# Optimization experiments

Measured on AMD Instinct MI355X. Metric: run time of the kernel, lower is better.

Reference implementation:

```python
import jax, jax.numpy as jnp
import numpy as np

MAX_REL = 64  # max_relative_position
LN_EPS = 1e-5


def _relative_positions(seq_len):
    r = jnp.arange(seq_len)
    rel = jnp.clip(r[None, :] - r[:, None], -MAX_REL, MAX_REL) + MAX_REL
    return rel  # [S, S] int32 in [0, 2*MAX_REL]


def setup_inputs() -> dict:
    key = jax.random.key(0)
    ks = jax.random.split(key, 8)
    B, S, H = 8, 1024, 128
    sd = 1.0 / np.sqrt(H)
    return {
        "x": jax.random.normal(ks[0], (B, S, H), jnp.float32),
        "Wq": jax.random.normal(ks[1], (H, H), jnp.float32) * sd,
        "bq": jnp.zeros((H,), jnp.float32),
        "Wk": jax.random.normal(ks[2], (H, H), jnp.float32) * sd,
        "bk": jnp.zeros((H,), jnp.float32),
        "Wv": jax.random.normal(ks[3], (H, H), jnp.float32) * sd,
        "bv": jnp.zeros((H,), jnp.float32),
        "rel_k": jax.random.normal(ks[4], (2 * MAX_REL + 1, H), jnp.float32),
        "rel_v": jax.random.normal(ks[5], (2 * MAX_REL + 1, H), jnp.float32),
        "Wo": jax.random.normal(ks[6], (H, H), jnp.float32) * sd,
        "bo": jnp.zeros((H,), jnp.float32),
        "gamma": jnp.ones((H,), jnp.float32),
        "beta": jnpp if False else jnp.zeros((H,), jnp.float32),
    }


def reference(x, Wq, bq, Wk, bk, Wv, bv, rel_k, rel_v, Wo, bo, gamma, beta):
    B, S, H = x.shape
    scale = jnp.sqrt(jnp.asarray(H, x.dtype))

    q = x @ Wq + bq  # [B,S,H]
    k = x @ Wk + bk
    v = x @ Wv + bv

    scores = jnp.einsum("bih,bjh->bij", q, k) / scale  # [B,S,S]

    relpos = _relative_positions(S)            # [S,S] int
    rk = rel_k[relpos]                          # [S,S,H] gather
    scores = scores + jnp.einsum("bih,ijh->bij", q, rk)

    attn = jax.nn.softmax(scores, axis=-1)      # dropout = identity (eval)

    ctx = jnp.einsum("bij,bjh->bih", attn, v)
    rv = rel_v[relpos]                          # [S,S,H] gather
    ctx = ctx + jnp.einsum("bij,ijh->bih", attn, rv)

    out = ctx @ Wo + bo

    # residual + LayerNorm
    y = out + x
    mu = jnp.mean(y, axis=-1, keepdims=True)
    var = jnp.mean(jnp.square(y - mu), axis=-1, keepdims=True)
    y = (y - mu) * jax.lax.rsqrt(var + LN_EPS) * gamma + beta
    return y, attn
```

## Files before the change

kernel.cpp:

```cpp
#include <hip/hip_runtime.h>

constexpr int Bn = 8, Sn = 1024, Hn = 128, Rn = 129;
constexpr float INV_SCALE = 0.088388347648318447f;
constexpr size_t YEL = (size_t)Bn * Sn * Hn;

typedef short bf16x8 __attribute__((ext_vector_type(8)));
typedef short v4s __attribute__((ext_vector_type(4)));
typedef float f32x4 __attribute__((ext_vector_type(4)));
typedef int v4i __attribute__((ext_vector_type(4)));

__device__ __forceinline__ float bf2f(short s) {
    unsigned u = ((unsigned)(unsigned short)s) << 16;
    float f; __builtin_memcpy(&f, &u, 4); return f;
}
__device__ __forceinline__ short f2bf(float f) {
    unsigned u; __builtin_memcpy(&u, &f, 4);
    unsigned r = (u + 0x7fffu + ((u >> 16) & 1u)) >> 16;
    return (short)(r & 0xffffu);
}

__device__ __forceinline__ void gll16(const short* g, short* l) {
    __builtin_amdgcn_global_load_lds(
        (const __attribute__((address_space(1))) void*)g,
        (__attribute__((address_space(3))) void*)l, 16, 0, 0);
}

__global__ __launch_bounds__(384) void build_tables(
    const float* __restrict__ rel_k, const float* __restrict__ rel_v,
    const float* __restrict__ Wo,
    short* __restrict__ relcat, short* __restrict__ BcatT)
{
    if (blockIdx.x < Rn) {
        const int p = blockIdx.x, c = threadIdx.x;
        const int j = (c < 256) ? (c & 127) : (c - 256);
        float v = rel_k[p * Hn + j];
        short h = f2bf(v);
        relcat[p * 384 + c] = (c < 256) ? h : f2bf(v - bf2f(h));
    } else {
        int idx = (blockIdx.x - Rn) * 384 + threadIdx.x;
        if (idx < 320 * 128) {
            int k = idx >> 7, n = idx & 127;
            float v;
            if (k < 128) v = Wo[k * Hn + n];
            else if (k < 257) {
                int p = k - 128; float a = 0.f;
                for (int h = 0; h < Hn; ++h) a += rel_v[p * Hn + h] * Wo[h * Hn + n];
                v = a;
            } else v = 0.f;
            BcatT[n * 320 + k] = f2bf(v);
        }
    }
}

__global__ __launch_bounds__(256) void proj(
    const float* __restrict__ X,
    const float* __restrict__ Wq, const float* __restrict__ bq,
    const float* __restrict__ Wk, const float* __restrict__ bk,
    const float* __restrict__ Wv, const float* __restrict__ bv,
    short* __restrict__ qcat, short* __restrict__ kh, short* __restrict__ vT)
{
    __shared__ float xs[64][128];
    __shared__ float wsm[32][128];
    const int tid = threadIdx.x;
    const int sel = blockIdx.y;
    const int row0 = blockIdx.x * 64;
    const float* W = (sel == 0) ? Wq : (sel == 1) ? Wk : Wv;
    const float* bias = (sel == 0) ? bq : (sel == 1) ? bk : bv;

#pragma unroll
    for (int it = 0; it < 8; ++it) {
        int u = tid + it * 256;
        int r = u >> 5, c4 = (u & 31) * 4;
        *(float4*)&xs[r][c4] = *(const float4*)(X + (size_t)(row0 + r) * 128 + c4);
    }

    const int rg = tid >> 5, cg = tid & 31;
    float acc[8][4] = {};
    for (int kc = 0; kc < 128; kc += 32) {
#pragma unroll
        for (int it = 0; it < 4; ++it) {
            int u = tid + it * 256;
            int kk = u >> 5, c4 = (u & 31) * 4;
            *(float4*)&wsm[kk][c4] = *(const float4*)(W + (size_t)(kc + kk) * 128 + c4);
        }
        __syncthreads();
#pragma unroll 8
        for (int kk = 0; kk < 32; ++kk) {
            float wv[4];
#pragma unroll
            for (int c = 0; c < 4; ++c) wv[c] = wsm[kk][cg + c * 32];
#pragma unroll
            for (int r = 0; r < 8; ++r) {
                float xv = xs[rg * 8 + r][kc + kk];
#pragma unroll
                for (int c = 0; c < 4; ++c) acc[r][c] += xv * wv[c];
            }
        }
        __syncthreads();
    }

#pragma unroll
    for (int c = 0; c < 4; ++c) {
        int col = cg + c * 32;
        float bv2 = bias[col];
#pragma unroll
        for (int r = 0; r < 8; ++r) {
            int row = row0 + rg * 8 + r;
            float v = acc[r][c] + bv2;
            short h = f2bf(v);
            if (sel == 0) {
                qcat[(size_t)row * 256 + col] = h;
                qcat[(size_t)row * 256 + 128 + col] = f2bf(v - bf2f(h));
            } else if (sel == 1) {
                kh[(size_t)row * 128 + col] = h;
            } else {
                int b = row >> 10, i = row & (Sn - 1);
                vT[(size_t)b * 131072 + (size_t)col * 1024 + i] = h;
            }
        }
    }
}

__global__ __launch_bounds__(512, 4) void fused_attn(
    const short* __restrict__ qcat, const short* __restrict__ kh,
    const short* __restrict__ vT, const short* __restrict__ relcat,
    const short* __restrict__ BcatT,
    const float* __restrict__ X, const float* __restrict__ bo,
    const float* __restrict__ gamma, const float* __restrict__ beta,
    float* __restrict__ attn_g, float* __restrict__ y_g)
{
    __shared__ __align__(16) char smem[78848];
    short* bufS = (short*)smem;
    short* Pb   = (short*)(smem + 32768);
    short* CtxA = (short*)(smem + 65792);
    float* QrL  = (float*)(smem + 65792);
    float* redM = (float*)(smem + 76800);
    float* redS = redM + 128;
    float* redL = redS + 128;
    float* redH = redL + 128;

    const int tid = threadIdx.x;
    const int w = tid >> 6, lane = tid & 63;
    const int quad = lane >> 4, l15 = lane & 15;
    const int lb = blockIdx.x + (blockIdx.z << 6);
    const int bz = lb & 7;
    const int row0 = (lb >> 3) << 4;
    const size_t grow0 = (size_t)bz * Sn + row0;

    const short* khb  = kh + (size_t)bz * Sn * 128;
    const short* vtb0 = vT + (size_t)bz * 131072;

    auto stage_kh = [&](int kt2) {
        const short* base = khb + (size_t)((kt2 >> 1) * 128) * 128 + (kt2 & 1) * 64;
        short* dst = bufS + (kt2 & 1) * 8192;
#pragma unroll
        for (int it = 0; it < 2; ++it) {
            int g = tid + it * 512;
            int r = g >> 3, c = g & 7;
            gll16(base + r * 128 + ((c ^ (r & 7)) * 8), dst + g * 8);
        }
    };
    auto stage_v = [&](int kc2) {
        const short* base = vtb0 + (kc2 >> 1) * 128 + (kc2 & 1) * 64;
        short* dst = bufS + (kc2 & 1) * 8192;
#pragma unroll
        for (int it = 0; it < 2; ++it) {
            int g = tid + it * 512;
            int r = g >> 3, c = g & 7;
            gll16(base + r * 1024 + ((c ^ (r & 7)) * 8), dst + g * 8);
        }
    };

    stage_kh(0);

    bf16x8 afr[4];
#pragma unroll
    for (int kk = 0; kk < 4; ++kk)
        afr[kk] = *(const bf16x8*)(qcat + (grow0 + l15) * 256 + kk * 32 + quad * 8);

    {
        const short* aq = qcat + (grow0 + l15) * 256;
        const short* br = relcat + (size_t)(w * 16 + l15) * 384;
        const short* br2 = relcat + (size_t)(128 + l15) * 384;
        f32x4 qacc = {};
        f32x4 qacc2 = {};
#pragma unroll
        for (int ks = 0; ks < 12; ++ks) {
            int koff = ks * 32 + quad * 8;
            int srcc = (koff >= 256) ? koff - 256 : koff;
            bf16x8 qa = *(const bf16x8*)(aq + srcc);
            bf16x8 qb = *(const bf16x8*)(br + ks * 32 + quad * 8);
            qacc = __builtin_amdgcn_mfma_f32_16x16x32_bf16(qa, qb, qacc, 0, 0, 0);
            if (w == 0) {
                bf16x8 qb2 = *(const bf16x8*)(br2 + ks * 32 + quad * 8);
                qacc2 = __builtin_amdgcn_mfma_f32_16x16x32_bf16(qa, qb2, qacc2, 0, 0, 0);
            }
        }
#pragma unroll
        for (int r = 0; r < 4; ++r)
            QrL[(quad * 4 + r) * 132 + w * 16 + l15] = qacc[r];
        if (w == 0 && l15 == 0) {
#pragma unroll
            for (int r = 0; r < 4; ++r)
                QrL[(quad * 4 + r) * 132 + 128] = qacc2[r];
        }
    }
    __syncthreads();

    f32x4 acc[8] = {};
#pragma unroll
    for (int kt2 = 0; kt2 < 16; ++kt2) {
        if (kt2 < 15) stage_kh(kt2 + 1);
        const short* hb = bufS + (kt2 & 1) * 8192;
        const int rb = w * 16 + l15;
#pragma unroll
        for (int kk = 0; kk < 2; ++kk) {
            int j = (kk * 4 + quad) ^ (l15 & 7);
            bf16x8 b = *(const bf16x8*)(hb + rb * 64 + j * 8);
            acc[kt2 >> 1] = __builtin_amdgcn_mfma_f32_16x16x32_bf16(
                afr[(kt2 & 1) * 2 + kk], b, acc[kt2 >> 1], 0, 0, 0);
        }
        __syncthreads();
    }

    stage_v(0);

    float mx[4];
#pragma unroll
    for (int r = 0; r < 4; ++r) {
        int lr = quad * 4 + r, i = row0 + lr;
        float m = -3.4e38f;
#pragma unroll
        for (int kt = 0; kt < 8; ++kt) {
            int col = kt * 128 + w * 16 + l15;
            int d = col - i; d = (d < -64) ? -64 : (d > 64 ? 64 : d);
            float v = acc[kt][r] * INV_SCALE + QrL[lr * 132 + d + 64];
            acc[kt][r] = v;
            m = fmaxf(m, v);
        }
#pragma unroll
        for (int msk = 1; msk < 16; msk <<= 1) m = fmaxf(m, __shfl_xor(m, msk));
        if (l15 == 0) redM[lr * 8 + w] = m;
    }
    __syncthreads();
#pragma unroll
    for (int r = 0; r < 4; ++r) {
        int lr = quad * 4 + r;
        float m = redM[lr * 8];
#pragma unroll
        for (int j = 1; j < 8; ++j) m = fmaxf(m, redM[lr * 8 + j]);
        mx[r] = m;
    }

#pragma unroll
    for (int r = 0; r < 4; ++r) {
        int lr = quad * 4 + r, i = row0 + lr;
        float s = 0.f, lo = 0.f, hi = 0.f;
#pragma unroll
        for (int kt = 0; kt < 8; ++kt) {
            float e = __expf(acc[kt][r] - mx[r]);
            acc[kt][r] = e;
            s += e;
            int col = kt * 128 + w * 16 + l15;
            lo += (col <= i - 64) ? e : 0.f;
            hi += (col >= i + 64) ? e : 0.f;
        }
#pragma unroll
        for (int msk = 1; msk < 16; msk <<= 1) {
            s += __shfl_xor(s, msk);
            lo += __shfl_xor(lo, msk);
            hi += __shfl_xor(hi, msk);
        }
        if (l15 == 0) { redS[lr * 8 + w] = s; redL[lr * 8 + w] = lo; redH[lr * 8 + w] = hi; }
    }
    __syncthreads();

#pragma unroll
    for (int r = 0; r < 4; ++r) {
        int lr = quad * 4 + r;
        float s = 0.f;
#pragma unroll
        for (int j = 0; j < 8; ++j) s += redS[lr * 8 + j];
        float inv = 1.0f / s;
#pragma unroll
        for (int kt = 0; kt < 8; ++kt) {
            int col = kt * 128 + w * 16 + l15;
            Pb[lr * 1032 + col] = f2bf(acc[kt][r] * inv);
        }
    }
    __syncthreads();

    {
        float* ab = attn_g + grow0 * Sn;
#pragma unroll
        for (int it = 0; it < 8; ++it) {
            int u = tid + it * 512;
            int r = u >> 8, c4 = (u & 255) * 4;
            v4s pv = *(const v4s*)&Pb[r * 1032 + c4];
            f32x4 o;
            o[0] = bf2f(pv[0]); o[1] = bf2f(pv[1]);
            o[2] = bf2f(pv[2]); o[3] = bf2f(pv[3]);
            __builtin_nontemporal_store(o, (f32x4*)(ab + (size_t)r * Sn + c4));
        }
    }

    f32x4 cacc = {};
#pragma unroll
    for (int kc2 = 0; kc2 < 16; ++kc2) {
        if (kc2 < 15) stage_v(kc2 + 1);
        const short* hb = bufS + (kc2 & 1) * 8192;
        const int rb = w * 16 + l15;
#pragma unroll
        for (int kk = 0; kk < 2; ++kk) {
            bf16x8 a = *(const bf16x8*)&Pb[l15 * 1032 + kc2 * 64 + kk * 32 + quad * 8];
            int j = (kk * 4 + quad) ^ (l15 & 7);
            bf16x8 b = *(const bf16x8*)(hb + rb * 64 + j * 8);
            cacc = __builtin_amdgcn_mfma_f32_16x16x32_bf16(a, b, cacc, 0, 0, 0);
        }
        __syncthreads();
    }

#pragma unroll
    for (int r = 0; r < 4; ++r)
        CtxA[(quad * 4 + r) * 344 + w * 16 + l15] = f2bf(cacc[r]);
#pragma unroll
    for (int rr = 0; rr < 2; ++rr) {
        int lr = w * 2 + rr, i = row0 + lr;
        float s = 0.f, lo = 0.f, hi = 0.f;
#pragma unroll
        for (int j = 0; j < 8; ++j) {
            s += redS[lr * 8 + j]; lo += redL[lr * 8 + j]; hi += redH[lr * 8 + j];
        }
        float inv = 1.0f / s;
        float v0;
        if (lane == 0) v0 = lo * inv;
        else { int c = i + lane - 64; v0 = (c >= 0 && c < Sn) ? bf2f(Pb[lr * 1032 + c]) : 0.f; }
        CtxA[lr * 344 + 128 + lane] = f2bf(v0);
        int c1 = i + lane;
        CtxA[lr * 344 + 192 + lane] = (c1 < Sn) ? Pb[lr * 1032 + c1] : (short)0;
        CtxA[lr * 344 + 256 + lane] = (lane == 0) ? f2bf(hi * inv) : (short)0;
    }
    __syncthreads();

    f32x4 yacc = {};
    const short* bcb = BcatT + (size_t)(w * 16 + l15) * 320;
#pragma unroll
    for (int ch = 0; ch < 3; ++ch) {
        const int nkk = (ch == 2) ? 2 : 4;
#pragma unroll
        for (int kk = 0; kk < 4; ++kk) {
            if (kk >= nkk) break;
            bf16x8 a = *(const bf16x8*)&CtxA[l15 * 344 + ch * 128 + kk * 32 + quad * 8];
            bf16x8 b = *(const bf16x8*)(bcb + ch * 128 + kk * 32 + quad * 8);
            yacc = __builtin_amdgcn_mfma_f32_16x16x32_bf16(a, b, yacc, 0, 0, 0);
        }
    }

    const int col = w * 16 + l15;
    const float bov = bo[col], gv = gamma[col], bev = beta[col];
    float vv[4];
#pragma unroll
    for (int r = 0; r < 4; ++r) {
        int lr = quad * 4 + r;
        vv[r] = yacc[r] + bov + X[(grow0 + lr) * 128 + col];
    }
#pragma unroll
    for (int r = 0; r < 4; ++r) {
        float s = vv[r];
#pragma unroll
        for (int msk = 1; msk < 16; msk <<= 1) s += __shfl_xor(s, msk);
        if (l15 == 0) redM[(quad * 4 + r) * 8 + w] = s;
    }
    __syncthreads();
    float mu[4];
#pragma unroll
    for (int r = 0; r < 4; ++r) {
        int lr = quad * 4 + r;
        float s = 0.f;
#pragma unroll
        for (int j = 0; j < 8; ++j) s += redM[lr * 8 + j];
        mu[r] = s * (1.f / 128.f);
    }
#pragma unroll
    for (int r = 0; r < 4; ++r) {
        float d = vv[r] - mu[r];
        float s = d * d;
#pragma unroll
        for (int msk = 1; msk < 16; msk <<= 1) s += __shfl_xor(s, msk);
        if (l15 == 0) redS[(quad * 4 + r) * 8 + w] = s;
    }
    __syncthreads();
#pragma unroll
    for (int r = 0; r < 4; ++r) {
        int lr = quad * 4 + r;
        float s = 0.f;
#pragma unroll
        for (int j = 0; j < 8; ++j) s += redS[lr * 8 + j];
        float inv = rsqrtf(s * (1.f / 128.f) + 1e-5f);
        float yv = (vv[r] - mu[r]) * inv * gv + bev;
        __builtin_nontemporal_store(yv, &y_g[(grow0 + lr) * 128 + col]);
    }
}

extern "C" void kernel_launch(void* const* d_in, const int* in_sizes, int n_in,
                              void* d_out, int out_size, void* d_ws, size_t ws_size,
                              hipStream_t stream) {
    const float* x     = (const float*)d_in[0];
    const float* Wq    = (const float*)d_in[1];
    const float* bq    = (const float*)d_in[2];
    const float* Wk    = (const float*)d_in[3];
    const float* bk    = (const float*)d_in[4];
    const float* Wv    = (const float*)d_in[5];
    const float* bv    = (const float*)d_in[6];
    const float* rel_k = (const float*)d_in[7];
    const float* rel_v = (const float*)d_in[8];
    const float* Wo    = (const float*)d_in[9];
    const float* bo    = (const float*)d_in[10];
    const float* gamma = (const float*)d_in[11];
    const float* beta  = (const float*)d_in[12];

    char* ws = (char*)d_ws;
    short* kh     = (short*)(ws + 0);
    short* vT     = (short*)(ws + 2097152);
    short* qcat   = (short*)(ws + 4194304);
    short* relcat = (short*)(ws + 8388608);
    short* BcatT  = (short*)(ws + 8519680);

    float* y_out = (float*)d_out;
    float* attn  = (float*)d_out + YEL;

    build_tables<<<dim3(Rn + 107), 384, 0, stream>>>(rel_k, rel_v, Wo, relcat, BcatT);
    proj<<<dim3(128, 3), 256, 0, stream>>>(x, Wq, bq, Wk, bk, Wv, bv, qcat, kh, vT);

    fused_attn<<<dim3(64, 1, Bn), 512, 0, stream>>>(
        qcat, kh, vT, relcat, BcatT, x, bo, gamma, beta, attn, y_out);
}
```

Baseline: 155.8 us.

## Use split-bf16 MFMA for QKV projection with pre-transposed weight tables

The QKV projection kernel now runs on bf16 MFMA instead of an FP32 scalar FMA loop. Accuracy is kept close to FP32 by splitting both x and W into high and low bf16 parts and issuing three MFMAs per tile. The weights are converted once into transposed hi/lo bf16 tables, built as extra blocks of the existing table-building kernel, and the projection reads them straight from global memory. This removes the weight staging through LDS and its barriers, at the cost of three times the MFMA work and a slight loss of precision compared with full FP32.

After: 154.7 us (median of 4 runs). Within noise of the previous version (-0.7%).

```diff
diff --git a/kernel.cpp b/kernel.cpp
--- a/kernel.cpp
+++ b/kernel.cpp
@@ -28,7 +28,10 @@
 __global__ __launch_bounds__(384) void build_tables(
     const float* __restrict__ rel_k, const float* __restrict__ rel_v,
     const float* __restrict__ Wo,
-    short* __restrict__ relcat, short* __restrict__ BcatT)
+    const float* __restrict__ Wq, const float* __restrict__ Wk,
+    const float* __restrict__ Wv,
+    short* __restrict__ relcat, short* __restrict__ BcatT,
+    short* __restrict__ wtab)
 {
     if (blockIdx.x < Rn) {
         const int p = blockIdx.x, c = threadIdx.x;
@@ -36,7 +39,7 @@
         float v = rel_k[p * Hn + j];
         short h = f2bf(v);
         relcat[p * 384 + c] = (c < 256) ? h : f2bf(v - bf2f(h));
-    } else {
+    } else if (blockIdx.x < Rn + 107) {
         int idx = (blockIdx.x - Rn) * 384 + threadIdx.x;
         if (idx < 320 * 128) {
             int k = idx >> 7, n = idx & 127;
@@ -49,23 +52,31 @@
             } else v = 0.f;
             BcatT[n * 320 + k] = f2bf(v);
         }
+    } else {
+        int idx = (blockIdx.x - Rn - 107) * 384 + threadIdx.x;
+        int sel = idx >> 14, rem = idx & 16383;
+        int n = rem >> 7, k = rem & 127;
+        const float* W = (sel == 0) ? Wq : (sel == 1) ? Wk : Wv;
+        float v = W[k * Hn + n];
+        short h = f2bf(v);
+        wtab[sel * 32768 + n * 128 + k] = h;
+        wtab[sel * 32768 + 16384 + n * 128 + k] = f2bf(v - bf2f(h));
     }
 }
 
 __global__ __launch_bounds__(256) void proj(
-    const float* __restrict__ X,
-    const float* __restrict__ Wq, const float* __restrict__ bq,
-    const float* __restrict__ Wk, const float* __restrict__ bk,
-    const float* __restrict__ Wv, const float* __restrict__ bv,
+    const float* __restrict__ X, const short* __restrict__ wtab,
+    const float* __restrict__ bq, const float* __restrict__ bk,
+    const float* __restrict__ bv,
     short* __restrict__ qcat, short* __restrict__ kh, short* __restrict__ vT)
 {
     __shared__ float xs[64][128];
-    __shared__ float wsm[32][128];
     const int tid = threadIdx.x;
     const int sel = blockIdx.y;
     const int row0 = blockIdx.x * 64;
-    const float* W = (sel == 0) ? Wq : (sel == 1) ? Wk : Wv;
     const float* bias = (sel == 0) ? bq : (sel == 1) ? bk : bv;
+    const short* wh = wtab + sel * 32768;
+    const short* wl = wh + 16384;
 
 #pragma unroll
     for (int it = 0; it < 8; ++it) {
@@ -73,40 +84,46 @@
         int r = u >> 5, c4 = (u & 31) * 4;
         *(float4*)&xs[r][c4] = *(const float4*)(X + (size_t)(row0 + r) * 128 + c4);
     }
-
-    const int rg = tid >> 5, cg = tid & 31;
-    float acc[8][4] = {};
-    for (int kc = 0; kc < 128; kc += 32) {
-#pragma unroll
-        for (int it = 0; it < 4; ++it) {
-            int u = tid + it * 256;
-            int kk = u >> 5, c4 = (u & 31) * 4;
-            *(float4*)&wsm[kk][c4] = *(const float4*)(W + (size_t)(kc + kk) * 128 + c4);
-        }
-        __syncthreads();
-#pragma unroll 8
-        for (int kk = 0; kk < 32; ++kk) {
-            float wv[4];
-#pragma unroll
-            for (int c = 0; c < 4; ++c) wv[c] = wsm[kk][cg + c * 32];
-#pragma unroll
-            for (int r = 0; r < 8; ++r) {
-                float xv = xs[rg * 8 + r][kc + kk];
-#pragma unroll
-                for (int c = 0; c < 4; ++c) acc[r][c] += xv * wv[c];
-            }
-        }
-        __syncthreads();
-    }
-
-#pragma unroll
-    for (int c = 0; c < 4; ++c) {
-        int col = cg + c * 32;
+    __syncthreads();
+
+    const int w = tid >> 6, lane = tid & 63;
+    const int quad = lane >> 4, l15 = lane & 15;
+
+    bf16x8 xh[4], xl[4];
+#pragma unroll
+    for (int kk = 0; kk < 4; ++kk) {
+#pragma unroll
+        for (int j = 0; j < 8; ++j) {
+            float v = xs[w * 16 + l15][kk * 32 + quad * 8 + j];
+            short h = f2bf(v);
+            xh[kk][j] = h;
+            xl[kk][j] = f2bf(v - bf2f(h));
+        }
+    }
+
+    f32x4 acc[8] = {};
+#pragma unroll
+    for (int nt = 0; nt < 8; ++nt) {
+        const short* bh = wh + (size_t)(nt * 16 + l15) * 128;
+        const short* bl = wl + (size_t)(nt * 16 + l15) * 128;
+#pragma unroll
+        for (int kk = 0; kk < 4; ++kk) {
+            bf16x8 bhf = *(const bf16x8*)(bh + kk * 32 + quad * 8);
+            bf16x8 blf = *(const bf16x8*)(bl + kk * 32 + quad * 8);
+            acc[nt] = __builtin_amdgcn_mfma_f32_16x16x32_bf16(xh[kk], bhf, acc[nt], 0, 0, 0);
+            acc[nt] = __builtin_amdgcn_mfma_f32_16x16x32_bf16(xh[kk], blf, acc[nt], 0, 0, 0);
+            acc[nt] = __builtin_amdgcn_mfma_f32_16x16x32_bf16(xl[kk], bhf, acc[nt], 0, 0, 0);
+        }
+    }
+
+#pragma unroll
+    for (int nt = 0; nt < 8; ++nt) {
+        int col = nt * 16 + l15;
         float bv2 = bias[col];
 #pragma unroll
-        for (int r = 0; r < 8; ++r) {
-            int row = row0 + rg * 8 + r;
-            float v = acc[r][c] + bv2;
+        for (int r = 0; r < 4; ++r) {
+            int row = row0 + w * 16 + quad * 4 + r;
+            float v = acc[nt][r] + bv2;
             short h = f2bf(v);
             if (sel == 0) {
                 qcat[(size_t)row * 256 + col] = h;
@@ -425,12 +442,14 @@
     short* qcat   = (short*)(ws + 4194304);
     short* relcat = (short*)(ws + 8388608);
     short* BcatT  = (short*)(ws + 8519680);
+    short* wtab   = (short*)(ws + 8650752);
 
     float* y_out = (float*)d_out;
     float* attn  = (float*)d_out + YEL;
 
-    build_tables<<<dim3(Rn + 107), 384, 0, stream>>>(rel_k, rel_v, Wo, relcat, BcatT);
-    proj<<<dim3(128, 3), 256, 0, stream>>>(x, Wq, bq, Wk, bk, Wv, bv, qcat, kh, vT);
+    build_tables<<<dim3(Rn + 107 + 128), 384, 0, stream>>>(
+        rel_k, rel_v, Wo, Wq, Wk, Wv, relcat, BcatT, wtab);
+    proj<<<dim3(128, 3), 256, 0, stream>>>(x, wtab, bq, bk, bv, qcat, kh, vT);
 
     fused_attn<<<dim3(64, 1, Bn), 512, 0, stream>>>(
         qcat, kh, vT, relcat, BcatT, x, bo, gamma, beta, attn, y_out);
```
